# Performance work log

Hardware: AMD Instinct MI355X
Metric: run time of the kernel (lower is better)

## Reference

```python
import jax, jax.numpy as jnp
import numpy as np

P, N, E, H = 8192, 32, 256, 8
D = E // H
CUT_A, CUT_B = 0.001, 0.005  # self.length_range = (0.001, 0.005, None, None)
SQRT3 = 1.7320508075688772


def _soft_square_cutoff(x):
    # smooth ramp 0->1 on [CUT_A, CUT_B], 0 below, 1 above (high-side ranges are None)
    t = jnp.clip((x - CUT_A) / (CUT_B - CUT_A), 0.0, 1.0)
    return 0.5 * (1.0 - jnp.cos(jnp.pi * t))


def setup_inputs() -> dict:
    key = jax.random.key(0)
    ks = jax.random.split(key, 16)
    s = 1.0 / np.sqrt(E)
    inp = {
        "query": jax.random.normal(ks[0], (P, E), jnp.float32),
        "key_x": jax.random.normal(ks[1], (P, E), jnp.float32),
        "value": jax.random.normal(ks[2], (P, E), jnp.float32),
        "index_pair": jax.random.randint(ks[3], (P, N), 0, P),
        "relative_atten_weights": jax.random.normal(ks[4], (P, N, H), jnp.float32),
        # lengths ~ N(0, 0.002*sqrt(3)) so they span the (0.001, 0.005) cutoff range
        "rpe_distance": jax.random.normal(ks[5], (P, N, 3), jnp.float32) * 0.002,
        "Wq": jax.random.normal(ks[6], (E, E), jnp.float32) * s,
        "bq": jnp.zeros((E,), jnp.float32),
        "Wk": jax.random.normal(ks[7], (E, E), jnp.float32) * s,
        "bk": jnp.zeros((E,), jnp.float32),
        "Wv": jax.random.normal(ks[8], (E, E), jnp.float32) * s,
        "bv": jnp.zeros((E,), jnp.float32),
        "Wg1": jax.random.normal(ks[9], (E, 3 * H), jnp.float32) * s,
        "bg1": jnp.zeros((3 * H,), jnp.float32),
        "Wg2": jax.random.normal(ks[10], (3 * H, 3 * H), jnp.float32) * (1.0 / np.sqrt(3 * H)),
        "bg2": jnp.zeros((3 * H,), jnp.float32),
    }
    return inp


def reference(query, key_x, value, index_pair, relative_atten_weights, rpe_distance,
              Wq, bq, Wk, bk, Wv, bv, Wg1, bg1, Wg2, bg2):
    # --- RPE spherical harmonics (irreps 1x0e+1x1e, component norm); keep l=1 part ([:,1:])
    rlen = jnp.linalg.norm(rpe_distance, axis=-1, keepdims=True)        # [P,N,1]
    unit = rpe_distance / jnp.maximum(rlen, 1e-12)                      # normalize=True
    cutoff = _soft_square_cutoff(rlen)                                  # nonscalar cutoff
    rpe_edge_sh = SQRT3 * unit * cutoff                                 # [P,N,3]

    # --- projections
    q = query @ Wq + bq                                                 # [P,E]
    k = key_x @ Wk + bk
    v = value @ Wv + bv

    # --- mapper_v6: per-edge gather of key/value rows
    k_g = k[index_pair]                                                 # [P,N,E]
    v_g = v[index_pair]                                                 # [P,N,E]

    # --- dot-product attention logits
    qh = q.reshape(P, H, D)
    kh = k_g.reshape(P, N, H, D)
    dot_atten = jnp.einsum('phd,pnhd->pnh', qh, kh)                     # [P,N,H]

    # --- MLP positional bias gated by spherical harmonics
    diff = k_g - q[:, None, :]                                          # [P,N,E]
    g = jax.nn.relu(diff @ Wg1 + bg1) @ Wg2 + bg2                       # [P,N,3H]
    g = g.reshape(P, N, H, 3)
    pos_atten = jnp.sum(g * rpe_edge_sh[:, :, None, :], axis=-1)        # [P,N,H]

    atten = (dot_atten + pos_atten + relative_atten_weights) / np.sqrt(D)
    atten = jax.nn.softmax(atten, axis=1)                               # over neighbors

    vh = v_g.reshape(P, N, H, D)
    out = jnp.einsum('pnh,pnhc->phc', atten, vh).reshape(P, E)
    return out
```

## Files before the change

kernel.cpp:

```cpp
#include <hip/hip_runtime.h>
#include <stdint.h>

typedef uint32_t u32;
typedef unsigned short u16;

#define LDT 40

typedef __bf16 bf16x8 __attribute__((ext_vector_type(8)));
typedef float  f32x4  __attribute__((ext_vector_type(4)));
typedef _Float16 h16x2 __attribute__((ext_vector_type(2)));

__device__ __forceinline__ float bf2f(u16 x) {
  union { float f; u32 u; } c; c.u = ((u32)x) << 16; return c.f;
}
__device__ __forceinline__ u16 f2bf(float f) {
  union { float f; u32 u; } c; c.f = f;
  u32 b = c.u;
  return (u16)((b + 0x7FFFu + ((b >> 16) & 1u)) >> 16);
}
__device__ __forceinline__ u32 pk2(float lo, float hi) {
  return (u32)f2bf(lo) | ((u32)f2bf(hi) << 16);
}
__device__ __forceinline__ u16 f2h(float f) {
  union { _Float16 h; u16 u; } c; c.h = (_Float16)f; return c.u;
}
__device__ __forceinline__ float h2f(u16 x) {
  union { _Float16 h; u16 u; } c; c.u = x; return (float)c.h;
}
__device__ __forceinline__ float fdot2u(u32 a, u32 b, float c) {
  union { u32 u; h16x2 h; } ua, ub; ua.u = a; ub.u = b;
#if __has_builtin(__builtin_amdgcn_fdot2)
  return __builtin_amdgcn_fdot2(ua.h, ub.h, c, false);
#else
  return c + (float)ua.h.x * (float)ub.h.x + (float)ua.h.y * (float)ub.h.y;
#endif
}

__global__ __launch_bounds__(256) void prep_transpose(
    const float* __restrict__ Wq, const float* __restrict__ Wk, const float* __restrict__ Wv,
    const float* __restrict__ Wg2,
    u16* __restrict__ WTq, u16* __restrict__ WTk, u16* __restrict__ WTv,
    u16* __restrict__ wg2bf)
{
  int z = blockIdx.z, bx = blockIdx.x, by = blockIdx.y;
  int x = threadIdx.x, y = threadIdx.y;
  if (z == 3) {
    if (bx || by) return;
    int t = y * 32 + x;
    for (int i = t; i < 1280; i += 256) {
      int j = i / 40, k = i % 40;
      float v = (j < 24 && k < 24) ? Wg2[(size_t)k * 24 + j] : 0.f;
      wg2bf[i] = f2bf(v);
    }
    return;
  }
  __shared__ u16 tile[32][33];
  const float* W  = (z == 0) ? Wq : (z == 1) ? Wk : Wv;
  u16*         WT = (z == 0) ? WTq : (z == 1) ? WTk : WTv;
  for (int yy = y; yy < 32; yy += 8)
    tile[yy][x] = f2bf(W[(size_t)(by * 32 + yy) * 256 + bx * 32 + x]);
  __syncthreads();
  for (int yy = y; yy < 32; yy += 8)
    WT[(size_t)(bx * 32 + yy) * 256 + by * 32 + x] = tile[x][yy];
}

__global__ __launch_bounds__(256) void prep_comb(
    const u16* __restrict__ WTq, const u16* __restrict__ WTk,
    const float* __restrict__ Wg1, const float* __restrict__ bg1,
    const float* __restrict__ bq, const float* __restrict__ bk,
    u16* __restrict__ CT, float* __restrict__ bcomb)
{
  int c = blockIdx.x, z = blockIdx.y;
  int t = threadIdx.x;
  const u16*   WT = (z == 0) ? WTq : WTk;
  const float* b  = (z == 0) ? bq : bk;

  float acc = 0.f;
#pragma unroll 8
  for (int e = 0; e < 256; e++)
    acc += bf2f(WT[(size_t)e * 256 + t]) * Wg1[(size_t)e * 24 + c];
  CT[(size_t)z * 8192 + (size_t)c * 256 + t] = f2bf(acc);

  __shared__ float red[256];
  red[t] = b[t] * Wg1[(size_t)t * 24 + c];
  __syncthreads();
  for (int s = 128; s > 0; s >>= 1) {
    if (t < s) red[t] += red[t + s];
    __syncthreads();
  }
  if (t == 0)
    bcomb[z * 24 + c] = red[0] - ((z == 0) ? bg1[c] : 0.f);
}

__global__ __launch_bounds__(256) void gemm_qkv(
    const float* __restrict__ Xq, const float* __restrict__ Xk, const float* __restrict__ Xv,
    const u16* __restrict__ WTq, const u16* __restrict__ WTk, const u16* __restrict__ WTv,
    const float* __restrict__ bq, const float* __restrict__ bk, const float* __restrict__ bv,
    const u16* __restrict__ CT, const float* __restrict__ bcomb,
    u16* __restrict__ Oq, u16* __restrict__ Ok, u16* __restrict__ Ov,
    u16* __restrict__ qadj, u16* __restrict__ kg1)
{
  int z = blockIdx.z;
  int nblk = blockIdx.y;
  if (nblk == 2 && z == 2) return;

  const float* X = (z == 0) ? Xq : (z == 1) ? Xk : Xv;
  int m0 = blockIdx.x * 128;
  int t = threadIdx.x;
  int lane = t & 63, wid = t >> 6;
  int fr = lane & 15, fg = lane >> 4;
  int sr = t >> 1;
  int sc = (t & 1) * 16;

  __shared__ __align__(16) u16 la[128 * LDT];
  __shared__ __align__(16) u16 lb[128 * LDT];

  if (nblk < 2) {
    const u16*   WT   = (z == 0) ? WTq : (z == 1) ? WTk : WTv;
    const float* bias = (z == 0) ? bq : (z == 1) ? bk : bv;
    u16*         O    = (z == 0) ? Oq : (z == 1) ? Ok : Ov;
    int n0 = nblk * 128;
    int wr = wid >> 1, wc = wid & 1;

    f32x4 acc[4][4];
#pragma unroll
    for (int i = 0; i < 4; i++)
#pragma unroll
      for (int j = 0; j < 4; j++) acc[i][j] = (f32x4){0.f, 0.f, 0.f, 0.f};

    for (int kt = 0; kt < 256; kt += 32) {
      const float4* ga = (const float4*)(X + (size_t)(m0 + sr) * 256 + kt + sc);
      float4 a0 = ga[0], a1 = ga[1], a2 = ga[2], a3 = ga[3];
      const uint4* gb = (const uint4*)(WT + (size_t)(n0 + sr) * 256 + kt + sc);
      uint4 b0 = gb[0], b1 = gb[1];

      uint4 wa0, wa1;
      wa0.x = pk2(a0.x, a0.y); wa0.y = pk2(a0.z, a0.w);
      wa0.z = pk2(a1.x, a1.y); wa0.w = pk2(a1.z, a1.w);
      wa1.x = pk2(a2.x, a2.y); wa1.y = pk2(a2.z, a2.w);
      wa1.z = pk2(a3.x, a3.y); wa1.w = pk2(a3.z, a3.w);

      __syncthreads();
      *(uint4*)&la[sr * LDT + sc]     = wa0;
      *(uint4*)&la[sr * LDT + sc + 8] = wa1;
      *(uint4*)&lb[sr * LDT + sc]     = b0;
      *(uint4*)&lb[sr * LDT + sc + 8] = b1;
      __syncthreads();

      bf16x8 af[4], bfr[4];
#pragma unroll
      for (int s = 0; s < 4; s++)
        af[s] = *(const bf16x8*)&la[(wr * 64 + s * 16 + fr) * LDT + fg * 8];
#pragma unroll
      for (int s = 0; s < 4; s++)
        bfr[s] = *(const bf16x8*)&lb[(wc * 64 + s * 16 + fr) * LDT + fg * 8];
#pragma unroll
      for (int i = 0; i < 4; i++)
#pragma unroll
        for (int j = 0; j < 4; j++)
          acc[i][j] = __builtin_amdgcn_mfma_f32_16x16x32_bf16(af[i], bfr[j], acc[i][j], 0, 0, 0);
    }

#pragma unroll
    for (int i = 0; i < 4; i++) {
      int rowb = m0 + wr * 64 + i * 16 + fg * 4;
#pragma unroll
      for (int j = 0; j < 4; j++) {
        int col = n0 + wc * 64 + j * 16 + fr;
        float bb = bias[col];
#pragma unroll
        for (int r = 0; r < 4; r++)
          O[(size_t)(rowb + r) * 256 + col] = f2h(acc[i][j][r] + bb);
      }
    }
  } else {
    const u16*   BT = CT + (size_t)z * 8192;
    const float* bc = bcomb + z * 24;
    u16*         O  = (z == 0) ? qadj : kg1;

    f32x4 acc[2][2];
#pragma unroll
    for (int i = 0; i < 2; i++)
#pragma unroll
      for (int j = 0; j < 2; j++) acc[i][j] = (f32x4){0.f, 0.f, 0.f, 0.f};

    for (int kt = 0; kt < 256; kt += 32) {
      const float4* ga = (const float4*)(X + (size_t)(m0 + sr) * 256 + kt + sc);
      float4 a0 = ga[0], a1 = ga[1], a2 = ga[2], a3 = ga[3];
      uint4 b0, b1;
      if (t < 64) {
        const uint4* gb = (const uint4*)(BT + (size_t)sr * 256 + kt + sc);
        b0 = gb[0]; b1 = gb[1];
      }
      uint4 wa0, wa1;
      wa0.x = pk2(a0.x, a0.y); wa0.y = pk2(a0.z, a0.w);
      wa0.z = pk2(a1.x, a1.y); wa0.w = pk2(a1.z, a1.w);
      wa1.x = pk2(a2.x, a2.y); wa1.y = pk2(a2.z, a2.w);
      wa1.z = pk2(a3.x, a3.y); wa1.w = pk2(a3.z, a3.w);

      __syncthreads();
      *(uint4*)&la[sr * LDT + sc]     = wa0;
      *(uint4*)&la[sr * LDT + sc + 8] = wa1;
      if (t < 64) {
        *(uint4*)&lb[sr * LDT + sc]     = b0;
        *(uint4*)&lb[sr * LDT + sc + 8] = b1;
      }
      __syncthreads();

      bf16x8 af[2], bfr[2];
#pragma unroll
      for (int s = 0; s < 2; s++)
        af[s] = *(const bf16x8*)&la[(wid * 32 + s * 16 + fr) * LDT + fg * 8];
#pragma unroll
      for (int s = 0; s < 2; s++)
        bfr[s] = *(const bf16x8*)&lb[(s * 16 + fr) * LDT + fg * 8];
#pragma unroll
      for (int i = 0; i < 2; i++)
#pragma unroll
        for (int j = 0; j < 2; j++)
          acc[i][j] = __builtin_amdgcn_mfma_f32_16x16x32_bf16(af[i], bfr[j], acc[i][j], 0, 0, 0);
    }

#pragma unroll
    for (int i = 0; i < 2; i++) {
      int rowb = m0 + wid * 32 + i * 16 + fg * 4;
#pragma unroll
      for (int j = 0; j < 2; j++) {
        int col = j * 16 + fr;
        if (col < 24) {
#pragma unroll
          for (int r = 0; r < 4; r++)
            O[(size_t)(rowb + r) * 32 + col] = f2h(acc[i][j][r] + bc[col]);
        }
      }
    }
  }
}

__global__ __launch_bounds__(256) void attn_logits(
    const u16* __restrict__ qb, const u16* __restrict__ kb,
    const u16* __restrict__ kg1g, const u16* __restrict__ qadjg,
    const int* __restrict__ ip, const float* __restrict__ raw,
    const float* __restrict__ rpe, const u16* __restrict__ wg2bf,
    const float* __restrict__ bg2g, u16* __restrict__ attg)
{
  int p = blockIdx.x, t = threadIdx.x;
  int lane = t & 63, w = t >> 6;
  int fr = lane & 15, fg = lane >> 4;
  int n = t >> 3, h = t & 7;

  __shared__ __align__(16) u16   wg2_s[32 * 40];
  __shared__ __align__(16) u16   kg1_s[32 * 40];
  __shared__              float qadj_s[24];
  __shared__              float bg2_s[24];
  __shared__              float sh_s[96];
  __shared__              float g_s[32 * 33];
  __shared__              float ev_s[256];
  __shared__              float is_s[8];

  int myidx = ip[(size_t)p * 32 + n];
  float rw = raw[(size_t)p * 256 + t];

  if ((t & 7) < 4)
    *(uint4*)&kg1_s[n * 40 + (t & 7) * 8] =
        *(const uint4*)(kg1g + (size_t)myidx * 32 + (t & 7) * 8);
  if (t < 160) *(uint4*)&wg2_s[t * 8] = ((const uint4*)wg2bf)[t];
  else if (t < 192) {
    int nn = t - 160;
    float x  = rpe[(size_t)p * 96 + nn * 3 + 0];
    float y  = rpe[(size_t)p * 96 + nn * 3 + 1];
    float z  = rpe[(size_t)p * 96 + nn * 3 + 2];
    float rl = sqrtf(x * x + y * y + z * z);
    float inv = 1.f / fmaxf(rl, 1e-12f);
    float tt2 = fminf(fmaxf((rl - 0.001f) * 250.f, 0.f), 1.f);
    float cut = 0.5f * (1.f - cosf(tt2 * 3.14159265358979f));
    float s3c = 1.7320508075688772f * inv * cut;
    sh_s[nn * 3 + 0] = x * s3c; sh_s[nn * 3 + 1] = y * s3c; sh_s[nn * 3 + 2] = z * s3c;
  }
  else if (t >= 192 && t < 216) qadj_s[t - 192] = h2f(qadjg[(size_t)p * 32 + (t - 192)]);
  else if (t >= 224 && t < 248) bg2_s[t - 224] = bg2g[t - 224];
  __syncthreads();

  {
    int mt = w & 1, jt = w >> 1;
    union { u32 u[4]; bf16x8 v; } a;
    if (fg < 3) {
      const u16*   kr = &kg1_s[(mt * 16 + fr) * 40 + fg * 8];
      const float* qr = &qadj_s[fg * 8];
      float x0 = fmaxf(h2f(kr[0]) - qr[0], 0.f), x1 = fmaxf(h2f(kr[1]) - qr[1], 0.f);
      float x2 = fmaxf(h2f(kr[2]) - qr[2], 0.f), x3 = fmaxf(h2f(kr[3]) - qr[3], 0.f);
      float x4 = fmaxf(h2f(kr[4]) - qr[4], 0.f), x5 = fmaxf(h2f(kr[5]) - qr[5], 0.f);
      float x6 = fmaxf(h2f(kr[6]) - qr[6], 0.f), x7 = fmaxf(h2f(kr[7]) - qr[7], 0.f);
      a.u[0] = pk2(x0, x1); a.u[1] = pk2(x2, x3);
      a.u[2] = pk2(x4, x5); a.u[3] = pk2(x6, x7);
    } else {
      a.u[0] = a.u[1] = a.u[2] = a.u[3] = 0;
    }
    bf16x8 b = *(const bf16x8*)&wg2_s[(jt * 16 + fr) * 40 + fg * 8];
    f32x4 g = (f32x4){0.f, 0.f, 0.f, 0.f};
    g = __builtin_amdgcn_mfma_f32_16x16x32_bf16(a.v, b, g, 0, 0, 0);
    int j = jt * 16 + fr;
    float bb = (j < 24) ? bg2_s[j] : 0.f;
    int e0 = mt * 16 + fg * 4;
#pragma unroll
    for (int r = 0; r < 4; r++)
      g_s[(e0 + r) * 33 + j] = g[r] + bb;
  }
  __syncthreads();

  float ev;
  {
    const uint4* kr = (const uint4*)(kb + (size_t)myidx * 256 + h * 32);
    const uint4* qr = (const uint4*)(qb + (size_t)p * 256 + h * 32);
    float dot = 0.f;
#pragma unroll
    for (int c = 0; c < 4; c++) {
      uint4 kw = kr[c], qw = qr[c];
      dot = fdot2u(kw.x, qw.x, dot);
      dot = fdot2u(kw.y, qw.y, dot);
      dot = fdot2u(kw.z, qw.z, dot);
      dot = fdot2u(kw.w, qw.w, dot);
    }
    float pos = g_s[n * 33 + h * 3 + 0] * sh_s[n * 3 + 0]
              + g_s[n * 33 + h * 3 + 1] * sh_s[n * 3 + 1]
              + g_s[n * 33 + h * 3 + 2] * sh_s[n * 3 + 2];
    ev = __expf((dot + pos + rw) * 0.17677669529663687f);
    ev_s[t] = ev;
  }
  __syncthreads();

  if (w == 0) {
    int hh = lane & 7, g4 = lane >> 3;
    float s = ev_s[(g4 * 4 + 0) * 8 + hh] + ev_s[(g4 * 4 + 1) * 8 + hh]
            + ev_s[(g4 * 4 + 2) * 8 + hh] + ev_s[(g4 * 4 + 3) * 8 + hh];
    s += __shfl_xor(s, 8, 64);
    s += __shfl_xor(s, 16, 64);
    s += __shfl_xor(s, 32, 64);
    if (lane < 8) is_s[hh] = 1.f / s;
  }
  __syncthreads();

  attg[(size_t)p * 256 + t] = f2h(ev * is_s[h]);
}

__global__ __launch_bounds__(256) void attn_pv(
    const u16* __restrict__ vb, const u16* __restrict__ attg,
    const int* __restrict__ ip, float* __restrict__ out)
{
  int t = threadIdx.x, wid = t >> 6, l = t & 63;
  int p = blockIdx.x * 4 + wid;
  __shared__ __align__(8) u16 att_s[4][256];
  __shared__ int idx_s[4][32];

  *(uint2*)&att_s[wid][l * 4] = *(const uint2*)(attg + (size_t)p * 256 + l * 4);
  if (l < 32) idx_s[wid][l] = ip[(size_t)p * 32 + l];

  int hh = l >> 3;
  float a0 = 0.f, a1 = 0.f, a2 = 0.f, a3 = 0.f;
#pragma unroll
  for (int n = 0; n < 32; n++) {
    float wt = h2f(att_s[wid][n * 8 + hh]);
    uint2 vv = *(const uint2*)(vb + (size_t)idx_s[wid][n] * 256 + l * 4);
    a0 += wt * h2f((u16)(vv.x & 0xFFFF));
    a1 += wt * h2f((u16)(vv.x >> 16));
    a2 += wt * h2f((u16)(vv.y & 0xFFFF));
    a3 += wt * h2f((u16)(vv.y >> 16));
  }
  float4 r; r.x = a0; r.y = a1; r.z = a2; r.w = a3;
  *(float4*)(out + (size_t)p * 256 + l * 4) = r;
}

extern "C" void kernel_launch(void* const* d_in, const int* in_sizes, int n_in,
                              void* d_out, int out_size, void* d_ws, size_t ws_size,
                              hipStream_t stream) {
  const float* query = (const float*)d_in[0];
  const float* key_x = (const float*)d_in[1];
  const float* value = (const float*)d_in[2];
  const int*   index_pair = (const int*)d_in[3];
  const float* raw  = (const float*)d_in[4];
  const float* rpe  = (const float*)d_in[5];
  const float* Wq = (const float*)d_in[6];
  const float* bq = (const float*)d_in[7];
  const float* Wk = (const float*)d_in[8];
  const float* bk = (const float*)d_in[9];
  const float* Wv = (const float*)d_in[10];
  const float* bv = (const float*)d_in[11];
  const float* Wg1 = (const float*)d_in[12];
  const float* bg1 = (const float*)d_in[13];
  const float* Wg2 = (const float*)d_in[14];
  const float* bg2 = (const float*)d_in[15];
  float* out = (float*)d_out;

  char* ws = (char*)d_ws;
  u16*   qbuf  = (u16*)(ws);
  u16*   kbuf  = (u16*)(ws + (4u << 20));
  u16*   vbuf  = (u16*)(ws + (8u << 20));
  u16*   attb  = (u16*)(ws + (12u << 20));
  u16*   qadj  = (u16*)(ws + (16u << 20));
  u16*   kg1   = (u16*)(ws + (16u << 20) + 524288);
  u16*   WTq   = (u16*)(ws + (17u << 20));
  u16*   WTk   = WTq + 65536;
  u16*   WTv   = WTk + 65536;
  u16*   CT    = WTv + 65536;
  float* bcomb = (float*)(CT + 16384);
  u16*   wg2bf = (u16*)(bcomb + 64);

  prep_transpose<<<dim3(8, 8, 4), dim3(32, 8, 1), 0, stream>>>(
      Wq, Wk, Wv, Wg2, WTq, WTk, WTv, wg2bf);
  prep_comb<<<dim3(24, 2), 256, 0, stream>>>(
      WTq, WTk, Wg1, bg1, bq, bk, CT, bcomb);
  gemm_qkv<<<dim3(64, 3, 3), 256, 0, stream>>>(
      query, key_x, value, WTq, WTk, WTv, bq, bk, bv, CT, bcomb,
      qbuf, kbuf, vbuf, qadj, kg1);
  attn_logits<<<8192, 256, 0, stream>>>(
      qbuf, kbuf, kg1, qadj, index_pair, raw, rpe, wg2bf, bg2, attb);
  attn_pv<<<2048, 256, 0, stream>>>(
      vbuf, attb, index_pair, out);
}
```

Baseline: 77.03 us.

## Replace fused Wq·Wg1 precompute with separate g1 GEMM on projected q/k, add nontemporal loads

```diff
diff --git a/kernel.cpp b/kernel.cpp
--- a/kernel.cpp
+++ b/kernel.cpp
@@ -9,6 +9,9 @@
 typedef __bf16 bf16x8 __attribute__((ext_vector_type(8)));
 typedef float  f32x4  __attribute__((ext_vector_type(4)));
 typedef _Float16 h16x2 __attribute__((ext_vector_type(2)));
+typedef u32    u32x4  __attribute__((ext_vector_type(4)));
+typedef u32    u32x2  __attribute__((ext_vector_type(2)));
+typedef float  f32x4v __attribute__((ext_vector_type(4)));
 
 __device__ __forceinline__ float bf2f(u16 x) {
   union { float f; u32 u; } c; c.u = ((u32)x) << 16; return c.f;
@@ -26,6 +29,9 @@
 }
 __device__ __forceinline__ float h2f(u16 x) {
   union { _Float16 h; u16 u; } c; c.u = x; return (float)c.h;
+}
+__device__ __forceinline__ u32 h2bf2(u32 w) {
+  return pk2(h2f((u16)(w & 0xFFFF)), h2f((u16)(w >> 16)));
 }
 __device__ __forceinline__ float fdot2u(u32 a, u32 b, float c) {
   union { u32 u; h16x2 h; } ua, ub; ua.u = a; ub.u = b;
@@ -38,9 +44,9 @@
 
 __global__ __launch_bounds__(256) void prep_transpose(
     const float* __restrict__ Wq, const float* __restrict__ Wk, const float* __restrict__ Wv,
-    const float* __restrict__ Wg2,
+    const float* __restrict__ Wg2, const float* __restrict__ Wg1,
     u16* __restrict__ WTq, u16* __restrict__ WTk, u16* __restrict__ WTv,
-    u16* __restrict__ wg2bf)
+    u16* __restrict__ wg2bf, u16* __restrict__ wg1T)
 {
   int z = blockIdx.z, bx = blockIdx.x, by = blockIdx.y;
   int x = threadIdx.x, y = threadIdx.y;
@@ -52,6 +58,10 @@
       float v = (j < 24 && k < 24) ? Wg2[(size_t)k * 24 + j] : 0.f;
       wg2bf[i] = f2bf(v);
     }
+    for (int j = 0; j < 24; j++)
+      wg1T[(size_t)j * 256 + t] = f2bf(Wg1[(size_t)t * 24 + j]);
+    for (int j = 24; j < 32; j++)
+      wg1T[(size_t)j * 256 + t] = 0;
     return;
   }
   __shared__ u16 tile[32][33];
@@ -64,47 +74,92 @@
     WT[(size_t)(bx * 32 + yy) * 256 + by * 32 + x] = tile[x][yy];
 }
 
-__global__ __launch_bounds__(256) void prep_comb(
-    const u16* __restrict__ WTq, const u16* __restrict__ WTk,
-    const float* __restrict__ Wg1, const float* __restrict__ bg1,
-    const float* __restrict__ bq, const float* __restrict__ bk,
-    u16* __restrict__ CT, float* __restrict__ bcomb)
-{
-  int c = blockIdx.x, z = blockIdx.y;
-  int t = threadIdx.x;
-  const u16*   WT = (z == 0) ? WTq : WTk;
-  const float* b  = (z == 0) ? bq : bk;
-
-  float acc = 0.f;
-#pragma unroll 8
-  for (int e = 0; e < 256; e++)
-    acc += bf2f(WT[(size_t)e * 256 + t]) * Wg1[(size_t)e * 24 + c];
-  CT[(size_t)z * 8192 + (size_t)c * 256 + t] = f2bf(acc);
-
-  __shared__ float red[256];
-  red[t] = b[t] * Wg1[(size_t)t * 24 + c];
-  __syncthreads();
-  for (int s = 128; s > 0; s >>= 1) {
-    if (t < s) red[t] += red[t + s];
-    __syncthreads();
-  }
-  if (t == 0)
-    bcomb[z * 24 + c] = red[0] - ((z == 0) ? bg1[c] : 0.f);
-}
-
 __global__ __launch_bounds__(256) void gemm_qkv(
     const float* __restrict__ Xq, const float* __restrict__ Xk, const float* __restrict__ Xv,
     const u16* __restrict__ WTq, const u16* __restrict__ WTk, const u16* __restrict__ WTv,
     const float* __restrict__ bq, const float* __restrict__ bk, const float* __restrict__ bv,
-    const u16* __restrict__ CT, const float* __restrict__ bcomb,
-    u16* __restrict__ Oq, u16* __restrict__ Ok, u16* __restrict__ Ov,
-    u16* __restrict__ qadj, u16* __restrict__ kg1)
+    u16* __restrict__ Oq, u16* __restrict__ Ok, u16* __restrict__ Ov)
 {
   int z = blockIdx.z;
-  int nblk = blockIdx.y;
-  if (nblk == 2 && z == 2) return;
-
-  const float* X = (z == 0) ? Xq : (z == 1) ? Xk : Xv;
+  const float* X    = (z == 0) ? Xq : (z == 1) ? Xk : Xv;
+  const u16*   WT   = (z == 0) ? WTq : (z == 1) ? WTk : WTv;
+  const float* bias = (z == 0) ? bq : (z == 1) ? bk : bv;
+  u16*         O    = (z == 0) ? Oq : (z == 1) ? Ok : Ov;
+
+  int m0 = blockIdx.x * 128;
+  int n0 = blockIdx.y * 128;
+  int t = threadIdx.x;
+  int lane = t & 63, wid = t >> 6;
+  int wr = wid >> 1, wc = wid & 1;
+  int fr = lane & 15, fg = lane >> 4;
+  int sr = t >> 1;
+  int sc = (t & 1) * 16;
+
+  __shared__ __align__(16) u16 la[128 * LDT];
+  __shared__ __align__(16) u16 lb[128 * LDT];
+
+  f32x4 acc[4][4];
+#pragma unroll
+  for (int i = 0; i < 4; i++)
+#pragma unroll
+    for (int j = 0; j < 4; j++) acc[i][j] = (f32x4){0.f, 0.f, 0.f, 0.f};
+
+  for (int kt = 0; kt < 256; kt += 32) {
+    const float4* ga = (const float4*)(X + (size_t)(m0 + sr) * 256 + kt + sc);
+    float4 a0 = ga[0], a1 = ga[1], a2 = ga[2], a3 = ga[3];
+    const uint4* gb = (const uint4*)(WT + (size_t)(n0 + sr) * 256 + kt + sc);
+    uint4 b0 = gb[0], b1 = gb[1];
+
+    uint4 wa0, wa1;
+    wa0.x = pk2(a0.x, a0.y); wa0.y = pk2(a0.z, a0.w);
+    wa0.z = pk2(a1.x, a1.y); wa0.w = pk2(a1.z, a1.w);
+    wa1.x = pk2(a2.x, a2.y); wa1.y = pk2(a2.z, a2.w);
+    wa1.z = pk2(a3.x, a3.y); wa1.w = pk2(a3.z, a3.w);
+
+    __syncthreads();
+    *(uint4*)&la[sr * LDT + sc]     = wa0;
+    *(uint4*)&la[sr * LDT + sc + 8] = wa1;
+    *(uint4*)&lb[sr * LDT + sc]     = b0;
+    *(uint4*)&lb[sr * LDT + sc + 8] = b1;
+    __syncthreads();
+
+    bf16x8 af[4], bfr[4];
+#pragma unroll
+    for (int s = 0; s < 4; s++)
+      af[s] = *(const bf16x8*)&la[(wr * 64 + s * 16 + fr) * LDT + fg * 8];
+#pragma unroll
+    for (int s = 0; s < 4; s++)
+      bfr[s] = *(const bf16x8*)&lb[(wc * 64 + s * 16 + fr) * LDT + fg * 8];
+#pragma unroll
+    for (int i = 0; i < 4; i++)
+#pragma unroll
+      for (int j = 0; j < 4; j++)
+        acc[i][j] = __builtin_amdgcn_mfma_f32_16x16x32_bf16(af[i], bfr[j], acc[i][j], 0, 0, 0);
+  }
+
+#pragma unroll
+  for (int i = 0; i < 4; i++) {
+    int rowb = m0 + wr * 64 + i * 16 + fg * 4;
+#pragma unroll
+    for (int j = 0; j < 4; j++) {
+      int col = n0 + wc * 64 + j * 16 + fr;
+      float bb = bias[col];
+#pragma unroll
+      for (int r = 0; r < 4; r++)
+        O[(size_t)(rowb + r) * 256 + col] = f2h(acc[i][j][r] + bb);
+    }
+  }
+}
+
+__global__ __launch_bounds__(256) void gemm_g1(
+    const u16* __restrict__ kbuf, const u16* __restrict__ qbuf,
+    const u16* __restrict__ wg1T, const float* __restrict__ bg1,
+    u16* __restrict__ kg1, u16* __restrict__ qadj)
+{
+  int z = blockIdx.y;
+  const u16* X = (z == 0) ? kbuf : qbuf;
+  u16*       O = (z == 0) ? kg1 : qadj;
+
   int m0 = blockIdx.x * 128;
   int t = threadIdx.x;
   int lane = t & 63, wid = t >> 6;
@@ -113,125 +168,62 @@
   int sc = (t & 1) * 16;
 
   __shared__ __align__(16) u16 la[128 * LDT];
-  __shared__ __align__(16) u16 lb[128 * LDT];
-
-  if (nblk < 2) {
-    const u16*   WT   = (z == 0) ? WTq : (z == 1) ? WTk : WTv;
-    const float* bias = (z == 0) ? bq : (z == 1) ? bk : bv;
-    u16*         O    = (z == 0) ? Oq : (z == 1) ? Ok : Ov;
-    int n0 = nblk * 128;
-    int wr = wid >> 1, wc = wid & 1;
-
-    f32x4 acc[4][4];
-#pragma unroll
-    for (int i = 0; i < 4; i++)
-#pragma unroll
-      for (int j = 0; j < 4; j++) acc[i][j] = (f32x4){0.f, 0.f, 0.f, 0.f};
-
-    for (int kt = 0; kt < 256; kt += 32) {
-      const float4* ga = (const float4*)(X + (size_t)(m0 + sr) * 256 + kt + sc);
-      float4 a0 = ga[0], a1 = ga[1], a2 = ga[2], a3 = ga[3];
-      const uint4* gb = (const uint4*)(WT + (size_t)(n0 + sr) * 256 + kt + sc);
-      uint4 b0 = gb[0], b1 = gb[1];
-
-      uint4 wa0, wa1;
-      wa0.x = pk2(a0.x, a0.y); wa0.y = pk2(a0.z, a0.w);
-      wa0.z = pk2(a1.x, a1.y); wa0.w = pk2(a1.z, a1.w);
-      wa1.x = pk2(a2.x, a2.y); wa1.y = pk2(a2.z, a2.w);
-      wa1.z = pk2(a3.x, a3.y); wa1.w = pk2(a3.z, a3.w);
-
-      __syncthreads();
-      *(uint4*)&la[sr * LDT + sc]     = wa0;
-      *(uint4*)&la[sr * LDT + sc + 8] = wa1;
+  __shared__ __align__(16) u16 lb[32 * LDT];
+
+  f32x4 acc[2][2];
+#pragma unroll
+  for (int i = 0; i < 2; i++)
+#pragma unroll
+    for (int j = 0; j < 2; j++) acc[i][j] = (f32x4){0.f, 0.f, 0.f, 0.f};
+
+  for (int kt = 0; kt < 256; kt += 32) {
+    const uint4* ga = (const uint4*)(X + (size_t)(m0 + sr) * 256 + kt + sc);
+    uint4 a0 = ga[0], a1 = ga[1];
+    uint4 b0, b1;
+    if (t < 64) {
+      const uint4* gb = (const uint4*)(wg1T + (size_t)sr * 256 + kt + sc);
+      b0 = gb[0]; b1 = gb[1];
+    }
+    uint4 wa0, wa1;
+    wa0.x = h2bf2(a0.x); wa0.y = h2bf2(a0.y);
+    wa0.z = h2bf2(a0.z); wa0.w = h2bf2(a0.w);
+    wa1.x = h2bf2(a1.x); wa1.y = h2bf2(a1.y);
+    wa1.z = h2bf2(a1.z); wa1.w = h2bf2(a1.w);
+
+    __syncthreads();
+    *(uint4*)&la[sr * LDT + sc]     = wa0;
+    *(uint4*)&la[sr * LDT + sc + 8] = wa1;
+    if (t < 64) {
       *(uint4*)&lb[sr * LDT + sc]     = b0;
       *(uint4*)&lb[sr * LDT + sc + 8] = b1;
-      __syncthreads();
-
-      bf16x8 af[4], bfr[4];
-#pragma unroll
-      for (int s = 0; s < 4; s++)
-        af[s] = *(const bf16x8*)&la[(wr * 64 + s * 16 + fr) * LDT + fg * 8];
-#pragma unroll
-      for (int s = 0; s < 4; s++)
-        bfr[s] = *(const bf16x8*)&lb[(wc * 64 + s * 16 + fr) * LDT + fg * 8];
-#pragma unroll
-      for (int i = 0; i < 4; i++)
-#pragma unroll
-        for (int j = 0; j < 4; j++)
-          acc[i][j] = __builtin_amdgcn_mfma_f32_16x16x32_bf16(af[i], bfr[j], acc[i][j], 0, 0, 0);
-    }
-
-#pragma unroll
-    for (int i = 0; i < 4; i++) {
-      int rowb = m0 + wr * 64 + i * 16 + fg * 4;
-#pragma unroll
-      for (int j = 0; j < 4; j++) {
-        int col = n0 + wc * 64 + j * 16 + fr;
-        float bb = bias[col];
+    }
+    __syncthreads();
+
+    bf16x8 af[2], bfr[2];
+#pragma unroll
+    for (int s = 0; s < 2; s++)
+      af[s] = *(const bf16x8*)&la[(wid * 32 + s * 16 + fr) * LDT + fg * 8];
+#pragma unroll
+    for (int s = 0; s < 2; s++)
+      bfr[s] = *(const bf16x8*)&lb[(s * 16 + fr) * LDT + fg * 8];
+#pragma unroll
+    for (int i = 0; i < 2; i++)
+#pragma unroll
+      for (int j = 0; j < 2; j++)
+        acc[i][j] = __builtin_amdgcn_mfma_f32_16x16x32_bf16(af[i], bfr[j], acc[i][j], 0, 0, 0);
+  }
+
+#pragma unroll
+  for (int i = 0; i < 2; i++) {
+    int rowb = m0 + wid * 32 + i * 16 + fg * 4;
+#pragma unroll
+    for (int j = 0; j < 2; j++) {
+      int col = j * 16 + fr;
+      if (col < 24) {
+        float sub = (z == 1) ? bg1[col] : 0.f;
 #pragma unroll
         for (int r = 0; r < 4; r++)
-          O[(size_t)(rowb + r) * 256 + col] = f2h(acc[i][j][r] + bb);
-      }
-    }
-  } else {
-    const u16*   BT = CT + (size_t)z * 8192;
-    const float* bc = bcomb + z * 24;
-    u16*         O  = (z == 0) ? qadj : kg1;
-
-    f32x4 acc[2][2];
-#pragma unroll
-    for (int i = 0; i < 2; i++)
-#pragma unroll
-      for (int j = 0; j < 2; j++) acc[i][j] = (f32x4){0.f, 0.f, 0.f, 0.f};
-
-    for (int kt = 0; kt < 256; kt += 32) {
-      const float4* ga = (const float4*)(X + (size_t)(m0 + sr) * 256 + kt + sc);
-      float4 a0 = ga[0], a1 = ga[1], a2 = ga[2], a3 = ga[3];
-      uint4 b0, b1;
-      if (t < 64) {
-        const uint4* gb = (const uint4*)(BT + (size_t)sr * 256 + kt + sc);
-        b0 = gb[0]; b1 = gb[1];
-      }
-      uint4 wa0, wa1;
-      wa0.x = pk2(a0.x, a0.y); wa0.y = pk2(a0.z, a0.w);
-      wa0.z = pk2(a1.x, a1.y); wa0.w = pk2(a1.z, a1.w);
-      wa1.x = pk2(a2.x, a2.y); wa1.y = pk2(a2.z, a2.w);
-      wa1.z = pk2(a3.x, a3.y); wa1.w = pk2(a3.z, a3.w);
-
-      __syncthreads();
-      *(uint4*)&la[sr * LDT + sc]     = wa0;
-      *(uint4*)&la[sr * LDT + sc + 8] = wa1;
-      if (t < 64) {
-        *(uint4*)&lb[sr * LDT + sc]     = b0;
-        *(uint4*)&lb[sr * LDT + sc + 8] = b1;
-      }
-      __syncthreads();
-
-      bf16x8 af[2], bfr[2];
-#pragma unroll
-      for (int s = 0; s < 2; s++)
-        af[s] = *(const bf16x8*)&la[(wid * 32 + s * 16 + fr) * LDT + fg * 8];
-#pragma unroll
-      for (int s = 0; s < 2; s++)
-        bfr[s] = *(const bf16x8*)&lb[(s * 16 + fr) * LDT + fg * 8];
-#pragma unroll
-      for (int i = 0; i < 2; i++)
-#pragma unroll
-        for (int j = 0; j < 2; j++)
-          acc[i][j] = __builtin_amdgcn_mfma_f32_16x16x32_bf16(af[i], bfr[j], acc[i][j], 0, 0, 0);
-    }
-
-#pragma unroll
-    for (int i = 0; i < 2; i++) {
-      int rowb = m0 + wid * 32 + i * 16 + fg * 4;
-#pragma unroll
-      for (int j = 0; j < 2; j++) {
-        int col = j * 16 + fr;
-        if (col < 24) {
-#pragma unroll
-          for (int r = 0; r < 4; r++)
-            O[(size_t)(rowb + r) * 32 + col] = f2h(acc[i][j][r] + bc[col]);
-        }
+          O[(size_t)(rowb + r) * 32 + col] = f2h(acc[i][j][r] - sub);
       }
     }
   }
@@ -259,7 +251,7 @@
   __shared__              float is_s[8];
 
   int myidx = ip[(size_t)p * 32 + n];
-  float rw = raw[(size_t)p * 256 + t];
+  float rw = __builtin_nontemporal_load(raw + (size_t)p * 256 + t);
 
   if ((t & 7) < 4)
     *(uint4*)&kg1_s[n * 40 + (t & 7) * 8] =
@@ -267,9 +259,9 @@
   if (t < 160) *(uint4*)&wg2_s[t * 8] = ((const uint4*)wg2bf)[t];
   else if (t < 192) {
     int nn = t - 160;
-    float x  = rpe[(size_t)p * 96 + nn * 3 + 0];
-    float y  = rpe[(size_t)p * 96 + nn * 3 + 1];
-    float z  = rpe[(size_t)p * 96 + nn * 3 + 2];
+    float x  = __builtin_nontemporal_load(rpe + (size_t)p * 96 + nn * 3 + 0);
+    float y  = __builtin_nontemporal_load(rpe + (size_t)p * 96 + nn * 3 + 1);
+    float z  = __builtin_nontemporal_load(rpe + (size_t)p * 96 + nn * 3 + 2);
     float rl = sqrtf(x * x + y * y + z * z);
     float inv = 1.f / fmaxf(rl, 1e-12f);
     float tt2 = fminf(fmaxf((rl - 0.001f) * 250.f, 0.f), 1.f);
@@ -277,7 +269,8 @@
     float s3c = 1.7320508075688772f * inv * cut;
     sh_s[nn * 3 + 0] = x * s3c; sh_s[nn * 3 + 1] = y * s3c; sh_s[nn * 3 + 2] = z * s3c;
   }
-  else if (t >= 192 && t < 216) qadj_s[t - 192] = h2f(qadjg[(size_t)p * 32 + (t - 192)]);
+  else if (t >= 192 && t < 216)
+    qadj_s[t - 192] = h2f(__builtin_nontemporal_load(qadjg + (size_t)p * 32 + (t - 192)));
   else if (t >= 224 && t < 248) bg2_s[t - 224] = bg2g[t - 224];
   __syncthreads();
 
@@ -310,16 +303,17 @@
 
   float ev;
   {
-    const uint4* kr = (const uint4*)(kb + (size_t)myidx * 256 + h * 32);
-    const uint4* qr = (const uint4*)(qb + (size_t)p * 256 + h * 32);
+    const uint4*  kr = (const uint4*)(kb + (size_t)myidx * 256 + h * 32);
+    const u32x4*  qr = (const u32x4*)(qb + (size_t)p * 256 + h * 32);
     float dot = 0.f;
 #pragma unroll
     for (int c = 0; c < 4; c++) {
-      uint4 kw = kr[c], qw = qr[c];
-      dot = fdot2u(kw.x, qw.x, dot);
-      dot = fdot2u(kw.y, qw.y, dot);
-      dot = fdot2u(kw.z, qw.z, dot);
-      dot = fdot2u(kw.w, qw.w, dot);
+      uint4 kw = kr[c];
+      u32x4 qw = __builtin_nontemporal_load(qr + c);
+      dot = fdot2u(kw.x, qw[0], dot);
+      dot = fdot2u(kw.y, qw[1], dot);
+      dot = fdot2u(kw.z, qw[2], dot);
+      dot = fdot2u(kw.w, qw[3], dot);
     }
     float pos = g_s[n * 33 + h * 3 + 0] * sh_s[n * 3 + 0]
               + g_s[n * 33 + h * 3 + 1] * sh_s[n * 3 + 1]
@@ -340,7 +334,7 @@
   }
   __syncthreads();
 
-  attg[(size_t)p * 256 + t] = f2h(ev * is_s[h]);
+  __builtin_nontemporal_store(f2h(ev * is_s[h]), attg + (size_t)p * 256 + t);
 }
 
 __global__ __launch_bounds__(256) void attn_pv(
@@ -352,7 +346,8 @@
   __shared__ __align__(8) u16 att_s[4][256];
   __shared__ int idx_s[4][32];
 
-  *(uint2*)&att_s[wid][l * 4] = *(const uint2*)(attg + (size_t)p * 256 + l * 4);
+  u32x2 aw = __builtin_nontemporal_load((const u32x2*)(attg + (size_t)p * 256 + l * 4));
+  *(u32x2*)&att_s[wid][l * 4] = aw;
   if (l < 32) idx_s[wid][l] = ip[(size_t)p * 32 + l];
 
   int hh = l >> 3;
@@ -366,8 +361,8 @@
     a2 += wt * h2f((u16)(vv.y & 0xFFFF));
     a3 += wt * h2f((u16)(vv.y >> 16));
   }
-  float4 r; r.x = a0; r.y = a1; r.z = a2; r.w = a3;
-  *(float4*)(out + (size_t)p * 256 + l * 4) = r;
+  f32x4v r; r[0] = a0; r[1] = a1; r[2] = a2; r[3] = a3;
+  __builtin_nontemporal_store(r, (f32x4v*)(out + (size_t)p * 256 + l * 4));
 }
 
 extern "C" void kernel_launch(void* const* d_in, const int* in_sizes, int n_in,
@@ -401,17 +396,15 @@
   u16*   WTq   = (u16*)(ws + (17u << 20));
   u16*   WTk   = WTq + 65536;
   u16*   WTv   = WTk + 65536;
-  u16*   CT    = WTv + 65536;
-  float* bcomb = (float*)(CT + 16384);
-  u16*   wg2bf = (u16*)(bcomb + 64);
+  u16*   wg2bf = WTv + 65536;
+  u16*   wg1T  = wg2bf + 1280;
 
   prep_transpose<<<dim3(8, 8, 4), dim3(32, 8, 1), 0, stream>>>(
-      Wq, Wk, Wv, Wg2, WTq, WTk, WTv, wg2bf);
-  prep_comb<<<dim3(24, 2), 256, 0, stream>>>(
-      WTq, WTk, Wg1, bg1, bq, bk, CT, bcomb);
-  gemm_qkv<<<dim3(64, 3, 3), 256, 0, stream>>>(
-      query, key_x, value, WTq, WTk, WTv, bq, bk, bv, CT, bcomb,
-      qbuf, kbuf, vbuf, qadj, kg1);
+      Wq, Wk, Wv, Wg2, Wg1, WTq, WTk, WTv, wg2bf, wg1T);
+  gemm_qkv<<<dim3(64, 2, 3), 256, 0, stream>>>(
+      query, key_x, value, WTq, WTk, WTv, bq, bk, bv, qbuf, kbuf, vbuf);
+  gemm_g1<<<dim3(64, 2), 256, 0, stream>>>(
+      kbuf, qbuf, wg1T, bg1, kg1, qadj);
   attn_logits<<<8192, 256, 0, stream>>>(
       qbuf, kbuf, kg1, qadj, index_pair, raw, rpe, wg2bf, bg2, attb);
   attn_pv<<<2048, 256, 0, stream>>>(
```

Measured after the change: 72.69 us. 5.6% less time.
